# Optimization experiments

Measured on AMD Instinct MI355X. Metric: run time of the kernel, lower is better.

## Reference

```python
import jax, jax.numpy as jnp
import numpy as np

B, N1, N2, D, H, DFF = 128, 256, 256, 256, 8, 1024
DH = D // H


def _ln(x, g, b, eps=1e-6):
    mu = jnp.mean(x, axis=-1, keepdims=True)
    var = jnp.mean(jnp.square(x - mu), axis=-1, keepdims=True)
    return g * (x - mu) / jnp.sqrt(var + eps) + b


def setup_inputs() -> dict:
    key = jax.random.key(0)
    ks = jax.random.split(key, 16)
    x1 = jax.random.normal(ks[0], (B, N1, D), jnp.float32)
    x2 = jax.random.normal(ks[1], (B, N2, D), jnp.float32)
    adj1 = (jax.random.uniform(ks[2], (B, N1, N1)) < 0.1).astype(jnp.float32)
    adj1 = jnp.maximum(adj1, jnp.eye(N1, dtype=jnp.float32)[None])
    mask1 = jnp.ones((B, N1), jnp.float32)
    mask2 = jnp.ones((B, N2), jnp.float32)
    s = 0.02
    Wq = jax.random.normal(ks[3], (D, D), jnp.float32) * s
    Wk = jax.random.normal(ks[4], (D, D), jnp.float32) * s
    Wv = jax.random.normal(ks[5], (D, D), jnp.float32) * s
    Wo = jax.random.normal(ks[6], (D, D), jnp.float32) * s
    W1 = jax.random.normal(ks[7], (D, DFF), jnp.float32) * s
    W2 = jax.random.normal(ks[8], (DFF, D), jnp.float32) * s
    return {
        "x1": x1, "adj1": adj1, "mask1": mask1, "x2": x2, "mask2": mask2,
        "Wq": Wq, "bq": jnp.zeros((D,), jnp.float32),
        "Wk": Wk, "bk": jnp.zeros((D,), jnp.float32),
        "Wv": Wv, "bv": jnp.zeros((D,), jnp.float32),
        "Wo": Wo, "bo": jnp.zeros((D,), jnp.float32),
        "W1": W1, "b1": jnp.zeros((DFF,), jnp.float32),
        "W2": W2, "b2": jnp.zeros((D,), jnp.float32),
        "g1": jnp.ones((D,), jnp.float32), "be1": jnp.zeros((D,), jnp.float32),
        "g2": jnp.ones((D,), jnp.float32), "be2": jnp.zeros((D,), jnp.float32),
    }


def reference(x1, adj1, mask1, x2, mask2, Wq, bq, Wk, bk, Wv, bv, Wo, bo,
              W1, b1, W2, b2, g1, be1, g2, be2):
    # Multi-head graph attention: self-attention on x1 masked by adjacency,
    # plus cross-attention from x1 to x2 masked by mask2 (PrismGATLayer).
    q = (x1 @ Wq + bq).reshape(B, N1, H, DH)
    k1 = (x1 @ Wk + bk).reshape(B, N1, H, DH)
    v1 = (x1 @ Wv + bv).reshape(B, N1, H, DH)
    k2 = (x2 @ Wk + bk).reshape(B, N2, H, DH)
    v2 = (x2 @ Wv + bv).reshape(B, N2, H, DH)
    scale = 1.0 / jnp.sqrt(jnp.float32(DH))

    s1 = jnp.einsum('bqhd,bkhd->bhqk', q, k1) * scale            # [B,H,N1,N1]
    m1 = adj1[:, None, :, :] * mask1[:, None, None, :]
    s1 = jnp.where(m1 > 0, s1, jnp.float32(-1e9))
    c1 = jnp.einsum('bhqk,bkhd->bqhd', jax.nn.softmax(s1, axis=-1), v1)

    s2 = jnp.einsum('bqhd,bkhd->bhqk', q, k2) * scale            # [B,H,N1,N2]
    s2 = jnp.where(mask2[:, None, None, :] > 0, s2, jnp.float32(-1e9))
    c2 = jnp.einsum('bhqk,bkhd->bqhd', jax.nn.softmax(s2, axis=-1), v2)

    attn = (c1 + c2).reshape(B, N1, D) @ Wo + bo
    out1 = _ln(x1 + attn, g1, be1)                               # dropout = identity (eval)
    ffn = jax.nn.relu(out1 @ W1 + b1) @ W2 + b2
    return _ln(out1 + ffn, g2, be2)
```

## Files before the change

### kernel.cpp

```cpp
#include <hip/hip_runtime.h>
#include <hip/hip_bf16.h>
#include <stdint.h>

#define B_   128
#define N1_  256
#define N2_  256
#define D_   256
#define H_   8
#define DH_  32
#define DFF_ 1024
#define M_   (B_*N1_)

typedef unsigned short ushortT;
typedef unsigned int   uintT;
typedef short bf16x8 __attribute__((ext_vector_type(8)));
typedef float f32x4  __attribute__((ext_vector_type(4)));

__device__ __forceinline__ float b2f(ushortT u){ return __uint_as_float(((uintT)u)<<16); }
__device__ __forceinline__ ushortT f2b(float f){
  uintT u = __float_as_uint(f);
  uintT r = (u + 0x7fffu + ((u>>16)&1u)) >> 16;
  return (ushortT)r;
}

__device__ __forceinline__ int sniff_wave(const ushortT* x){
  const int e = (x[threadIdx.x & 63] >> 7) & 0xff;
  const unsigned long long bad = __ballot(e < 100 || e > 135);
  return __popcll(bad) >= 12;
}
__device__ __forceinline__ float ldin(const void* p, size_t i, int f32){
  return f32 ? ((const float*)p)[i] : b2f(((const ushortT*)p)[i]);
}

__global__ __launch_bounds__(256) void conv_bf16_kernel(
    const void* __restrict__ X, ushortT* __restrict__ Y, int n8,
    const ushortT* __restrict__ sniffp)
{
  const int in_f32 = sniff_wave(sniffp);
  int i = blockIdx.x * 256 + threadIdx.x;
  if (i >= n8) return;
  size_t base = (size_t)i * 8;
  if (in_f32) {
    float4 a = *(const float4*)((const float*)X + base);
    float4 b = *(const float4*)((const float*)X + base + 4);
    ushort4 o0, o1;
    o0.x=f2b(a.x); o0.y=f2b(a.y); o0.z=f2b(a.z); o0.w=f2b(a.w);
    o1.x=f2b(b.x); o1.y=f2b(b.y); o1.z=f2b(b.z); o1.w=f2b(b.w);
    *(ushort4*)(Y + base)     = o0;
    *(ushort4*)(Y + base + 4) = o1;
  } else {
    *(uint4*)(Y + base) = *(const uint4*)((const ushortT*)X + base);
  }
}

__global__ __launch_bounds__(256) void transpose_w_kernel(
    const void* __restrict__ W, ushortT* __restrict__ Wt, int K, int N,
    const ushortT* __restrict__ sniffp)
{
  const int in_f32 = sniff_wave(sniffp);
  __shared__ float t[32][33];
  const int tx = threadIdx.x & 31, ty = threadIdx.x >> 5;
  const int n0 = blockIdx.x * 32, k0 = blockIdx.y * 32;
  #pragma unroll
  for (int i = 0; i < 4; i++)
    t[ty + 8*i][tx] = ldin(W, (size_t)(k0 + ty + 8*i) * N + n0 + tx, in_f32);
  __syncthreads();
  #pragma unroll
  for (int i = 0; i < 4; i++)
    Wt[(size_t)(n0 + ty + 8*i) * K + k0 + tx] = f2b(t[tx][ty + 8*i]);
}

__global__ __launch_bounds__(256) void transpose_b_kernel(
    const ushortT* __restrict__ V, ushortT* __restrict__ Vt)
{
  __shared__ ushortT t[32][33];
  const int b = blockIdx.z;
  const int d0 = blockIdx.x * 32, t0 = blockIdx.y * 32;
  const int tx = threadIdx.x & 31, ty = threadIdx.x >> 5;
  const size_t base = (size_t)b * 65536;
  #pragma unroll
  for (int i = 0; i < 4; i++)
    t[ty + 8*i][tx] = V[base + (size_t)(t0 + ty + 8*i) * 256 + d0 + tx];
  __syncthreads();
  #pragma unroll
  for (int i = 0; i < 4; i++)
    Vt[base + (size_t)(d0 + ty + 8*i) * 256 + t0 + tx] = t[tx][ty + 8*i];
}

__global__ __launch_bounds__(256) void pack_adj_kernel(
    const void* __restrict__ ADJ, uintT* __restrict__ AB,
    const ushortT* __restrict__ sniffp)
{
  const int in_f32 = sniff_wave(sniffp);
  const int idx = blockIdx.x * 256 + threadIdx.x;
  const size_t base = (size_t)(idx >> 3) * 256 + (size_t)(idx & 7) * 32;
  uintT bits = 0;
  if (in_f32) {
    const float* ap = (const float*)ADJ + base;
    #pragma unroll
    for (int j4 = 0; j4 < 8; j4++) {
      float4 v = *(const float4*)(ap + j4 * 4);
      bits |= (v.x > 0.f ? 1u : 0u) << (j4 * 4 + 0);
      bits |= (v.y > 0.f ? 1u : 0u) << (j4 * 4 + 1);
      bits |= (v.z > 0.f ? 1u : 0u) << (j4 * 4 + 2);
      bits |= (v.w > 0.f ? 1u : 0u) << (j4 * 4 + 3);
    }
  } else {
    const ushortT* ap = (const ushortT*)ADJ + base;
    #pragma unroll
    for (int j = 0; j < 32; j++)
      bits |= (b2f(ap[j]) > 0.f ? 1u : 0u) << j;
  }
  AB[idx] = bits;
}

__global__ __launch_bounds__(256) void pack_mask_kernel(
    const void* __restrict__ M1, const void* __restrict__ M2,
    uintT* __restrict__ MW, const ushortT* __restrict__ sniffp)
{
  const int in_f32 = sniff_wave(sniffp);
  const int idx = blockIdx.x * 256 + threadIdx.x;
  const int src = idx >> 10;
  const void* MP = src ? M2 : M1;
  const size_t base = (size_t)((idx >> 3) & 127) * 256 + (size_t)(idx & 7) * 32;
  uintT bits = 0;
  #pragma unroll
  for (int j = 0; j < 32; j++)
    bits |= (ldin(MP, base + j, in_f32) > 0.f ? 1u : 0u) << j;
  MW[idx] = bits;
}

__global__ __launch_bounds__(256) void gemm128_kernel(
    const ushortT* __restrict__ A, const ushortT* __restrict__ Bt,
    const void* __restrict__ bias, ushortT* __restrict__ C,
    int M, int N, int K, int relu, const ushortT* __restrict__ sniffp)
{
  __shared__ ushortT Al[128 * 40];
  __shared__ ushortT Bl[128 * 40];

  const int tid = threadIdx.x;
  const int in_f32 = sniff_wave(sniffp);
  const int wave = tid >> 6, lane = tid & 63;
  const int l15 = lane & 15, l4 = lane >> 4;
  const int wm = wave & 1, wn = wave >> 1;
  const int row0 = blockIdx.x * 128, col0 = blockIdx.y * 128;
  const int m0 = wm * 64, n0 = wn * 64;

  f32x4 acc[4][4];
  #pragma unroll
  for (int i = 0; i < 4; i++)
    #pragma unroll
    for (int j = 0; j < 4; j++) acc[i][j] = (f32x4)0.f;

  const int sr = tid >> 2;
  const int sk = (tid & 3) * 8;

  const ushortT* Ap = &A[(size_t)(row0 + sr) * K + sk];
  const ushortT* Bp = &Bt[(size_t)(col0 + sr) * K + sk];
  const size_t step64 = (size_t)64 * K;

  uint4 a0 = *(const uint4*)Ap;
  uint4 a1 = *(const uint4*)(Ap + step64);
  uint4 b0 = *(const uint4*)Bp;
  uint4 b1 = *(const uint4*)(Bp + step64);

  for (int kt = 0; kt < K; kt += 32) {
    __syncthreads();
    *(uint4*)&Al[sr * 40 + sk]        = a0;
    *(uint4*)&Al[(sr + 64) * 40 + sk] = a1;
    *(uint4*)&Bl[sr * 40 + sk]        = b0;
    *(uint4*)&Bl[(sr + 64) * 40 + sk] = b1;
    __syncthreads();
    if (kt + 32 < K) {
      a0 = *(const uint4*)(Ap + kt + 32);
      a1 = *(const uint4*)(Ap + step64 + kt + 32);
      b0 = *(const uint4*)(Bp + kt + 32);
      b1 = *(const uint4*)(Bp + step64 + kt + 32);
    }
    bf16x8 af[4], bf[4];
    #pragma unroll
    for (int mt = 0; mt < 4; mt++)
      af[mt] = *(const bf16x8*)&Al[(m0 + mt * 16 + l15) * 40 + l4 * 8];
    #pragma unroll
    for (int nt = 0; nt < 4; nt++)
      bf[nt] = *(const bf16x8*)&Bl[(n0 + nt * 16 + l15) * 40 + l4 * 8];
    #pragma unroll
    for (int mt = 0; mt < 4; mt++)
      #pragma unroll
      for (int nt = 0; nt < 4; nt++)
        acc[mt][nt] = __builtin_amdgcn_mfma_f32_16x16x32_bf16(af[mt], bf[nt], acc[mt][nt], 0, 0, 0);
  }

  #pragma unroll
  for (int nt = 0; nt < 4; nt++) {
    int col = col0 + n0 + nt * 16 + l15;
    float bb = ldin(bias, col, in_f32);
    #pragma unroll
    for (int mt = 0; mt < 4; mt++) {
      #pragma unroll
      for (int r = 0; r < 4; r++) {
        float v = acc[mt][nt][r] + bb;
        if (relu) v = fmaxf(v, 0.f);
        int row = row0 + m0 + mt * 16 + l4 * 4 + r;
        C[(size_t)row * N + col] = f2b(v);
      }
    }
  }
}

#define LNROWS 4
__global__ __launch_bounds__(256) void add_ln_kernel(
    const void* __restrict__ X, const ushortT* __restrict__ Y,
    const void* __restrict__ gamma, const void* __restrict__ beta,
    void* __restrict__ out, const ushortT* __restrict__ sniffp,
    int x_dyn, int store_dyn)
{
  const int in_f32 = sniff_wave(sniffp);
  const int xf32 = x_dyn ? in_f32 : 0;
  const int lane = threadIdx.x & 63;
  const int gw = blockIdx.x * 4 + (threadIdx.x >> 6);
  const int d0 = lane * 4;

  float g[4], be[4];
  if (in_f32) {
    float4 gv = *(const float4*)((const float*)gamma + d0);
    float4 bv = *(const float4*)((const float*)beta  + d0);
    g[0]=gv.x; g[1]=gv.y; g[2]=gv.z; g[3]=gv.w;
    be[0]=bv.x; be[1]=bv.y; be[2]=bv.z; be[3]=bv.w;
  } else {
    ushort4 gv = *(const ushort4*)((const ushortT*)gamma + d0);
    ushort4 bv = *(const ushort4*)((const ushortT*)beta  + d0);
    g[0]=b2f(gv.x); g[1]=b2f(gv.y); g[2]=b2f(gv.z); g[3]=b2f(gv.w);
    be[0]=b2f(bv.x); be[1]=b2f(bv.y); be[2]=b2f(bv.z); be[3]=b2f(bv.w);
  }

  const int row0 = gw * LNROWS;

  float v[LNROWS][4];
  #pragma unroll
  for (int rr = 0; rr < LNROWS; rr++) {
    const size_t base = (size_t)(row0 + rr) * D_ + d0;
    const ushort4 yv = *(const ushort4*)(Y + base);
    if (xf32) {
      float4 xv = *(const float4*)((const float*)X + base);
      v[rr][0] = xv.x + b2f(yv.x); v[rr][1] = xv.y + b2f(yv.y);
      v[rr][2] = xv.z + b2f(yv.z); v[rr][3] = xv.w + b2f(yv.w);
    } else {
      ushort4 xv = *(const ushort4*)((const ushortT*)X + base);
      v[rr][0] = b2f(xv.x) + b2f(yv.x); v[rr][1] = b2f(xv.y) + b2f(yv.y);
      v[rr][2] = b2f(xv.z) + b2f(yv.z); v[rr][3] = b2f(xv.w) + b2f(yv.w);
    }
  }

  #pragma unroll
  for (int rr = 0; rr < LNROWS; rr++) {
    float s = (v[rr][0] + v[rr][1]) + (v[rr][2] + v[rr][3]);
    float q = (v[rr][0]*v[rr][0] + v[rr][1]*v[rr][1])
            + (v[rr][2]*v[rr][2] + v[rr][3]*v[rr][3]);
    #pragma unroll
    for (int off = 1; off < 64; off <<= 1) {
      s += __shfl_xor(s, off, 64);
      q += __shfl_xor(q, off, 64);
    }
    const float mu   = s * (1.f / D_);
    const float var  = q * (1.f / D_) - mu * mu;
    const float rstd = rsqrtf(var + 1e-6f);
    const size_t base = (size_t)(row0 + rr) * D_ + d0;
    if (store_dyn && in_f32) {
      float4 o;
      o.x = g[0]*(v[rr][0]-mu)*rstd + be[0];
      o.y = g[1]*(v[rr][1]-mu)*rstd + be[1];
      o.z = g[2]*(v[rr][2]-mu)*rstd + be[2];
      o.w = g[3]*(v[rr][3]-mu)*rstd + be[3];
      *(float4*)((float*)out + base) = o;
    } else {
      ushort4 o;
      o.x = f2b(g[0]*(v[rr][0]-mu)*rstd + be[0]);
      o.y = f2b(g[1]*(v[rr][1]-mu)*rstd + be[1]);
      o.z = f2b(g[2]*(v[rr][2]-mu)*rstd + be[2]);
      o.w = f2b(g[3]*(v[rr][3]-mu)*rstd + be[3]);
      *(ushort4*)((ushortT*)out + base) = o;
    }
  }
}

__global__ __launch_bounds__(256) void attn_mfma_kernel(
    ushortT* __restrict__ QC,
    const ushortT* __restrict__ K1, const ushortT* __restrict__ K2,
    const ushortT* __restrict__ V1t, const ushortT* __restrict__ V2t,
    const uintT* __restrict__ AB, const uintT* __restrict__ MW)
{
  const float scale = 0.17677669529663687f;
  const int qt = blockIdx.x, h = blockIdx.y, b = blockIdx.z;
  const int q0 = qt * 64;
  const int tid = threadIdx.x;
  const int wave = tid >> 6, lane = tid & 63;
  const int l15 = lane & 15, l4 = lane >> 4;

  __shared__ __align__(16) ushortT P[64][268];
  __shared__ uintT adjl[64][8];
  __shared__ uintT mwv[2][8];

  const size_t bh = (size_t)b * 256;

  {
    const uintT* src = AB + ((size_t)(b * 256 + q0)) * 8;
    uintT* fl = &adjl[0][0];
    *(uint2*)&fl[tid * 2] = *(const uint2*)&src[tid * 2];
    if (tid < 16) mwv[tid >> 3][tid & 7] = MW[((tid >> 3) * 128 + b) * 8 + (tid & 7)];
  }

  const bf16x8 af = *(const bf16x8*)&QC[(bh + q0 + wave*16 + l15) * 256 + h*32 + l4*8];
  __syncthreads();

  const int prow = wave * 16 + l15;

  f32x4 acc0 = (f32x4)0.f, acc1 = (f32x4)0.f;

  #pragma unroll 1
  for (int src = 0; src < 2; src++) {
    const ushortT* Kp  = src ? K2  : K1;
    const ushortT* Vtp = src ? V2t : V1t;

    float rsum = 0.f;
    #pragma unroll 1
    for (int c = 0; c < 4; c++) {
      bf16x8 kf[4];
      #pragma unroll
      for (int j = 0; j < 4; j++)
        kf[j] = *(const bf16x8*)&Kp[(bh + (c*4 + j)*16 + l15) * 256 + h*32 + l4*8];
      #pragma unroll
      for (int j = 0; j < 4; j++) {
        const int nt = c*4 + j;
        const f32x4 s4 = __builtin_amdgcn_mfma_f32_16x16x32_bf16(kf[j], af, (f32x4)0.f, 0, 0, 0);
        const int tb = nt*16 + l4*4;
        const int sh = tb & 31;
        uintT bits = mwv[src][nt >> 1] >> sh;
        if (src == 0) bits &= adjl[prow][nt >> 1] >> sh;
        const float e0 = (bits & 1u) ? __expf(s4[0] * scale) : 0.f;
        const float e1 = (bits & 2u) ? __expf(s4[1] * scale) : 0.f;
        const float e2 = (bits & 4u) ? __expf(s4[2] * scale) : 0.f;
        const float e3 = (bits & 8u) ? __expf(s4[3] * scale) : 0.f;
        rsum += (e0 + e1) + (e2 + e3);
        ushort4 pw;
        pw.x = f2b(e0); pw.y = f2b(e1); pw.z = f2b(e2); pw.w = f2b(e3);
        *(ushort4*)&P[prow][tb] = pw;
      }
    }
    rsum += __shfl_xor(rsum, 16, 64);
    rsum += __shfl_xor(rsum, 32, 64);
    const float rv = 1.f / rsum;
    float rvr[4];
    #pragma unroll
    for (int r = 0; r < 4; r++) rvr[r] = __shfl(rv, l4*4 + r, 64);

    f32x4 o0 = (f32x4)0.f, o1 = (f32x4)0.f;
    #pragma unroll
    for (int kt = 0; kt < 8; kt++) {
      const bf16x8 ap = *(const bf16x8*)&P[prow][kt*32 + l4*8];
      const bf16x8 v0 = *(const bf16x8*)&Vtp[(bh + h*32 + l15) * 256 + kt*32 + l4*8];
      const bf16x8 v1 = *(const bf16x8*)&Vtp[(bh + h*32 + 16 + l15) * 256 + kt*32 + l4*8];
      o0 = __builtin_amdgcn_mfma_f32_16x16x32_bf16(ap, v0, o0, 0, 0, 0);
      o1 = __builtin_amdgcn_mfma_f32_16x16x32_bf16(ap, v1, o1, 0, 0, 0);
    }
    #pragma unroll
    for (int r = 0; r < 4; r++) { acc0[r] += o0[r] * rvr[r]; acc1[r] += o1[r] * rvr[r]; }
  }

  #pragma unroll
  for (int r = 0; r < 4; r++) {
    const int row = (int)(bh + q0 + wave*16 + l4*4 + r);
    QC[(size_t)row * 256 + h*32 + l15]      = f2b(acc0[r]);
    QC[(size_t)row * 256 + h*32 + 16 + l15] = f2b(acc1[r]);
  }
}

extern "C" void kernel_launch(void* const* d_in, const int* in_sizes, int n_in,
                              void* d_out, int out_size, void* d_ws, size_t ws_size,
                              hipStream_t stream) {
  const void* x1    = d_in[0];
  const void* adj1  = d_in[1];
  const void* mask1 = d_in[2];
  const void* x2    = d_in[3];
  const void* mask2 = d_in[4];
  const void* Wq = d_in[5];  const void* bq = d_in[6];
  const void* Wk = d_in[7];  const void* bk = d_in[8];
  const void* Wv = d_in[9];  const void* bv = d_in[10];
  const void* Wo = d_in[11]; const void* bo = d_in[12];
  const void* W1 = d_in[13]; const void* b1 = d_in[14];
  const void* W2 = d_in[15]; const void* b2 = d_in[16];
  const void* g1 = d_in[17]; const void* be1= d_in[18];
  const void* g2 = d_in[19]; const void* be2= d_in[20];
  const ushortT* sniffp = (const ushortT*)x1;

  ushortT* ws = (ushortT*)d_ws;
  const size_t SZ = (size_t)M_ * D_;
  ushortT* S0 = ws;
  ushortT* S1 = ws + SZ;
  ushortT* S2 = ws + 2*SZ;
  ushortT* S3 = ws + 3*SZ;
  ushortT* S4 = ws + 4*SZ;
  ushortT* S5 = ws + 5*SZ;
  ushortT* dOut = (ushortT*)d_out;

  ushortT* Wkt = S1;
  ushortT* Wvt = S1 + 65536;
  ushortT* Wqt = S1 + 131072;
  ushortT* Wot = S2;
  ushortT* W1t = dOut;
  ushortT* W2t = dOut + 262144;
  uintT* AB = (uintT*)(dOut + 9437184);
  uintT* MWp = AB + 262144;

  dim3 blk(256);
  dim3 gGemmD(M_/128, D_/128);
  dim3 gGemmF(M_/128, DFF_/128);
  dim3 gT256(8, 8);
  dim3 gTB(8, 8, B_);
  const int n8 = (int)(SZ / 8);

  pack_adj_kernel<<<dim3(1024), blk, 0, stream>>>(adj1, AB, sniffp);
  pack_mask_kernel<<<dim3(8), blk, 0, stream>>>(mask1, mask2, MWp, sniffp);

  conv_bf16_kernel<<<dim3((n8+255)/256), blk, 0, stream>>>(x2, S2, n8, sniffp);
  transpose_w_kernel<<<gT256, blk, 0, stream>>>(Wk, Wkt, D_, D_, sniffp);
  transpose_w_kernel<<<gT256, blk, 0, stream>>>(Wv, Wvt, D_, D_, sniffp);
  transpose_w_kernel<<<gT256, blk, 0, stream>>>(Wq, Wqt, D_, D_, sniffp);

  gemm128_kernel<<<gGemmD, blk, 0, stream>>>(S2, Wkt, bk, S3, M_, D_, D_, 0, sniffp);
  gemm128_kernel<<<gGemmD, blk, 0, stream>>>(S2, Wvt, bv, S4, M_, D_, D_, 0, sniffp);

  conv_bf16_kernel<<<dim3((n8+255)/256), blk, 0, stream>>>(x1, S0, n8, sniffp);

  gemm128_kernel<<<gGemmD, blk, 0, stream>>>(S0, Wkt, bk, S2, M_, D_, D_, 0, sniffp);
  gemm128_kernel<<<gGemmD, blk, 0, stream>>>(S0, Wvt, bv, dOut, M_, D_, D_, 0, sniffp);
  gemm128_kernel<<<gGemmD, blk, 0, stream>>>(S0, Wqt, bq, S0, M_, D_, D_, 0, sniffp);

  transpose_b_kernel<<<gTB, blk, 0, stream>>>(S4, S1);
  transpose_b_kernel<<<gTB, blk, 0, stream>>>(dOut, S4);
  transpose_w_kernel<<<dim3(DFF_/32, D_/32), blk, 0, stream>>>(W1, W1t, D_, DFF_, sniffp);
  transpose_w_kernel<<<dim3(D_/32, DFF_/32), blk, 0, stream>>>(W2, W2t, DFF_, D_, sniffp);

  attn_mfma_kernel<<<dim3(N1_/64, H_, B_), blk, 0, stream>>>(
      S0, S2, S3, S4, S1, AB, MWp);

  transpose_w_kernel<<<gT256, blk, 0, stream>>>(Wo, Wot, D_, D_, sniffp);
  gemm128_kernel<<<gGemmD, blk, 0, stream>>>(S0, Wot, bo, S3, M_, D_, D_, 0, sniffp);

  add_ln_kernel<<<dim3(M_/16), blk, 0, stream>>>(x1, S3, g1, be1, S0, sniffp, 1, 0);

  gemm128_kernel<<<gGemmF, blk, 0, stream>>>(S0, W1t, b1, S1, M_, DFF_, D_, 1, sniffp);

  gemm128_kernel<<<gGemmD, blk, 0, stream>>>(S1, W2t, b2, S5, M_, D_, DFF_, 0, sniffp);

  add_ln_kernel<<<dim3(M_/16), blk, 0, stream>>>(S0, S5, g2, be2, d_out, sniffp, 0, 1);
}
```

Before: 519.0 us.

## Swizzle block order for XCD locality and tighten attention softmax inner loop

Remaps linear block IDs in the GEMM and attention kernels so that consecutive blocks landing on the same XCD share operand tiles (same batch/head or rows), improving L2 reuse across the MI355X chiplets. In the attention kernel it also hoists adjacency and mask words into registers, packs bf16 conversion with v_cvt_pk_bf16_f32 inline asm, changes the LDS row padding from 268 to 264, and raises wave priority around the PV MFMA loop. The swizzle assumes grid sizes are divisible by 8 and gridDim.y is a power of two. The new padding may change LDS bank conflicts.

```diff
diff --git a/kernel.cpp b/kernel.cpp
--- a/kernel.cpp
+++ b/kernel.cpp
@@ -143,7 +143,13 @@
   const int wave = tid >> 6, lane = tid & 63;
   const int l15 = lane & 15, l4 = lane >> 4;
   const int wm = wave & 1, wn = wave >> 1;
-  const int row0 = blockIdx.x * 128, col0 = blockIdx.y * 128;
+
+  const int lin = blockIdx.x + gridDim.x * blockIdx.y;
+  const int chunk = (gridDim.x * gridDim.y) >> 3;
+  const int gsw = (lin & 7) * chunk + (lin >> 3);
+  const int ylog = 31 - __clz(gridDim.y);
+  const int bx = gsw >> ylog, by = gsw & (gridDim.y - 1);
+  const int row0 = bx * 128, col0 = by * 128;
   const int m0 = wm * 64, n0 = wn * 64;
 
   f32x4 acc[4][4];
@@ -291,13 +297,15 @@
     const uintT* __restrict__ AB, const uintT* __restrict__ MW)
 {
   const float scale = 0.17677669529663687f;
-  const int qt = blockIdx.x, h = blockIdx.y, b = blockIdx.z;
+  const int lin = blockIdx.x + (blockIdx.y << 2) + (blockIdx.z << 5);
+  const int gsw = (lin & 7) * 512 + (lin >> 3);
+  const int b = gsw >> 5, h = (gsw >> 2) & 7, qt = gsw & 3;
   const int q0 = qt * 64;
   const int tid = threadIdx.x;
   const int wave = tid >> 6, lane = tid & 63;
   const int l15 = lane & 15, l4 = lane >> 4;
 
-  __shared__ __align__(16) ushortT P[64][268];
+  __shared__ __align__(16) ushortT P[64][264];
   __shared__ uintT adjl[64][8];
   __shared__ uintT mwv[2][8];
 
@@ -315,12 +323,20 @@
 
   const int prow = wave * 16 + l15;
 
+  uintT adjr[8];
+  #pragma unroll
+  for (int w = 0; w < 8; w++) adjr[w] = adjl[prow][w];
+
   f32x4 acc0 = (f32x4)0.f, acc1 = (f32x4)0.f;
 
   #pragma unroll 1
   for (int src = 0; src < 2; src++) {
     const ushortT* Kp  = src ? K2  : K1;
     const ushortT* Vtp = src ? V2t : V1t;
+
+    uintT mww[8];
+    #pragma unroll
+    for (int w = 0; w < 8; w++) mww[w] = mwv[src][w];
 
     float rsum = 0.f;
     #pragma unroll 1
@@ -335,16 +351,18 @@
         const f32x4 s4 = __builtin_amdgcn_mfma_f32_16x16x32_bf16(kf[j], af, (f32x4)0.f, 0, 0, 0);
         const int tb = nt*16 + l4*4;
         const int sh = tb & 31;
-        uintT bits = mwv[src][nt >> 1] >> sh;
-        if (src == 0) bits &= adjl[prow][nt >> 1] >> sh;
+        uintT bits = mww[nt >> 1] >> sh;
+        if (src == 0) bits &= adjr[nt >> 1] >> sh;
         const float e0 = (bits & 1u) ? __expf(s4[0] * scale) : 0.f;
         const float e1 = (bits & 2u) ? __expf(s4[1] * scale) : 0.f;
         const float e2 = (bits & 4u) ? __expf(s4[2] * scale) : 0.f;
         const float e3 = (bits & 8u) ? __expf(s4[3] * scale) : 0.f;
         rsum += (e0 + e1) + (e2 + e3);
-        ushort4 pw;
-        pw.x = f2b(e0); pw.y = f2b(e1); pw.z = f2b(e2); pw.w = f2b(e3);
-        *(ushort4*)&P[prow][tb] = pw;
+        uintT pk01, pk23;
+        asm("v_cvt_pk_bf16_f32 %0, %1, %2" : "=v"(pk01) : "v"(e0), "v"(e1));
+        asm("v_cvt_pk_bf16_f32 %0, %1, %2" : "=v"(pk23) : "v"(e2), "v"(e3));
+        uint2 pw; pw.x = pk01; pw.y = pk23;
+        *(uint2*)&P[prow][tb] = pw;
       }
     }
     rsum += __shfl_xor(rsum, 16, 64);
@@ -355,6 +373,7 @@
     for (int r = 0; r < 4; r++) rvr[r] = __shfl(rv, l4*4 + r, 64);
 
     f32x4 o0 = (f32x4)0.f, o1 = (f32x4)0.f;
+    __builtin_amdgcn_s_setprio(1);
     #pragma unroll
     for (int kt = 0; kt < 8; kt++) {
       const bf16x8 ap = *(const bf16x8*)&P[prow][kt*32 + l4*8];
@@ -363,6 +382,7 @@
       o0 = __builtin_amdgcn_mfma_f32_16x16x32_bf16(ap, v0, o0, 0, 0, 0);
       o1 = __builtin_amdgcn_mfma_f32_16x16x32_bf16(ap, v1, o1, 0, 0, 0);
     }
+    __builtin_amdgcn_s_setprio(0);
     #pragma unroll
     for (int r = 0; r < 4; r++) { acc0[r] += o0[r] * rvr[r]; acc1[r] += o1[r] * rvr[r]; }
   }
```

Result: faster. 492.1 us (-5.2%).
